# Optimization experiments

Measured on AMD Instinct MI355X. Metric: run time of the kernel, lower is better.

## Reference

```python
import jax, jax.numpy as jnp
import numpy as np

DIM = 1024
N_HEADS = 16
HEAD_DIM = DIM // N_HEADS


def setup_inputs() -> dict:
    key = jax.random.key(0)
    k_x, k_qkv, k_out = jax.random.split(key, 3)
    B, T = 4, 2048
    x = jax.random.normal(k_x, (B, T, DIM), dtype=jnp.float32)
    W_qkv = jax.random.normal(k_qkv, (DIM, 3 * DIM), dtype=jnp.float32) * 0.02
    b_qkv = jnp.zeros((3 * DIM,), dtype=jnp.float32)
    W_out = jax.random.normal(k_out, (DIM, DIM), dtype=jnp.float32) * 0.02
    b_out = jnp.zeros((DIM,), dtype=jnp.float32)
    return {"x": x, "W_qkv": W_qkv, "b_qkv": b_qkv, "W_out": W_out, "b_out": b_out}


def reference(x, W_qkv, b_qkv, W_out, b_out):
    B, T, C = x.shape
    qkv = x @ W_qkv + b_qkv  # (B, T, 3C)
    q, k, v = jnp.split(qkv, 3, axis=-1)
    # (B, H, T, D)
    q = q.reshape(B, T, N_HEADS, HEAD_DIM).transpose(0, 2, 1, 3)
    k = k.reshape(B, T, N_HEADS, HEAD_DIM).transpose(0, 2, 1, 3)
    v = v.reshape(B, T, N_HEADS, HEAD_DIM).transpose(0, 2, 1, 3)
    scale = 1.0 / jnp.sqrt(jnp.asarray(HEAD_DIM, dtype=x.dtype))
    scores = jnp.einsum('bhqd,bhkd->bhqk', q, k) * scale  # (B, H, T, T)
    causal = jnp.tril(jnp.ones((T, T), dtype=bool))  # True = allowed
    scores = jnp.where(causal, scores, jnp.asarray(-jnp.inf, dtype=scores.dtype))
    attn = jax.nn.softmax(scores, axis=-1)
    out = jnp.einsum('bhqk,bhkd->bhqd', attn, v)  # (B, H, T, D)
    out = out.transpose(0, 2, 1, 3).reshape(B, T, C)
    return out @ W_out + b_out
```

## Files before the change

kernel.cpp:

```cpp
#include <hip/hip_runtime.h>
#include <hip/hip_bf16.h>
#include <cstdint>
#include <cstddef>

#define DIM   1024
#define NH    16
#define HD    64
#define BB    4
#define TT    2048

typedef __attribute__((ext_vector_type(8))) short bf16x8;
typedef __attribute__((ext_vector_type(4))) short bf16x4;
typedef __attribute__((ext_vector_type(4))) float f32x4;
typedef __attribute__((ext_vector_type(4))) unsigned short u16x4;
typedef unsigned short u16;
typedef unsigned int u32;

#define NEG_INF (-__builtin_inff())
#define QSCALE 0.18033688011110543f
#define AS1 __attribute__((address_space(1)))
#define AS3 __attribute__((address_space(3)))

static __device__ __forceinline__ u16 f2bf(float f) {
  union { float f; unsigned u; } v; v.f = f;
  return (u16)((v.u + 0x7FFFu + ((v.u >> 16) & 1u)) >> 16);
}

static __device__ __forceinline__ u16 bfbits(float a) {
  union { __hip_bfloat16 h; u16 u; } c; c.h = __float2bfloat16(a); return c.u;
}
static __device__ __forceinline__ u32 pk_bf16(float a, float b) {
  return (u32)bfbits(a) | ((u32)bfbits(b) << 16);
}

static __device__ __forceinline__ float exp2_fast(float x) {
  float r;
  asm("v_exp_f32 %0, %1" : "=v"(r) : "v"(x));
  return r;
}

static __device__ __forceinline__ bf16x4 tr16(u32 byte_addr) {
  bf16x4 d;
  asm volatile("ds_read_b64_tr_b16 %0, %1" : "=v"(d) : "v"(byte_addr));
  return d;
}

#define MFMA16(A, B, C) __builtin_amdgcn_mfma_f32_16x16x32_bf16(A, B, C, 0, 0, 0)

__global__ __launch_bounds__(256) void k_cvt(const float* __restrict__ in,
                                             u16* __restrict__ out, int n4) {
  int i = blockIdx.x * 256 + threadIdx.x;
  if (i >= n4) return;
  float4 v = reinterpret_cast<const float4*>(in)[i];
  u16x4 o = { f2bf(v.x), f2bf(v.y), f2bf(v.z), f2bf(v.w) };
  *reinterpret_cast<u16x4*>(out + (size_t)i * 4) = o;
}

__global__ __launch_bounds__(256) void k_transpose(const float* __restrict__ in,
                                                   u16* __restrict__ out,
                                                   int R, int C) {
  __shared__ float tile[32][33];
  int bx = blockIdx.x * 32;
  int by = blockIdx.y * 32;
  int tx = threadIdx.x & 31, ty = threadIdx.x >> 5;
  #pragma unroll
  for (int i = 0; i < 32; i += 8)
    tile[ty + i][tx] = in[(size_t)(by + ty + i) * C + bx + tx];
  __syncthreads();
  #pragma unroll
  for (int i = 0; i < 32; i += 8)
    out[(size_t)(bx + ty + i) * R + by + tx] = f2bf(tile[tx][ty + i]);
}

template <int OUT_BF16>
__global__ __launch_bounds__(512, 2) void k_gemm8p(const u16* __restrict__ A,
                                                   const u16* __restrict__ Bt,
                                                   const float* __restrict__ bias,
                                                   u16* __restrict__ Cb,
                                                   float* __restrict__ Cf,
                                                   int M, int N, int K,
                                                   int scale_cols, float scale,
                                                   int nbx) {
  __shared__ __align__(16) char lds[131072];

  const int tid = threadIdx.x;
  const int nwg = gridDim.x;
  const int qq = nwg >> 3, rm = nwg & 7;
  const int xcd = blockIdx.x & 7, lidx = blockIdx.x >> 3;
  const int swz = (xcd < rm ? xcd * (qq + 1) : rm * (qq + 1) + (xcd - rm) * qq) + lidx;
  const int m0 = (swz / nbx) * 256, n0 = (swz % nbx) * 128;

  const int w = tid >> 6, lane = tid & 63;
  const int g = lane >> 4, r = lane & 15;
  const int wm = w >> 1, wn = w & 1;

  f32x4 acc[4][4] = {};
  const int KT = K >> 6;

  auto stageH = [&](char* base, const u16* src, int grow0, int kt) {
    #pragma unroll
    for (int i = 0; i < 2; ++i) {
      int o = (tid + i * 512) * 16;
      int l = o ^ (((o >> 9) & 1) << 5);
      int row = (l >> 6) & 127, ks = l >> 13, kb = l & 63;
      const u16* gp = src + (size_t)(grow0 + row) * K + kt * 64 + ks * 32 + (kb >> 1);
      __builtin_amdgcn_global_load_lds((const AS1 void*)gp, (AS3 void*)(base + o), 16, 0, 0);
    }
  };
  auto stageA = [&](int t) {
    char* ab = lds + (t % 3) * 32768;
    stageH(ab, A, m0, t);
    stageH(ab + 16384, A, m0 + 128, t);
  };
  auto stageB = [&](int t) {
    stageH(lds + 98304 + (t & 1) * 16384, Bt, n0, t);
  };

  auto ldAf = [&](int t, int f, bf16x8 (&dst)[2]) {
    const char* base = lds + (t % 3) * 32768 + (wm >> 1) * 16384;
    int rowb = ((wm & 1) * 64 + f * 16 + r) * 64 + g * 16;
    #pragma unroll
    for (int ks = 0; ks < 2; ++ks) {
      int l = ks * 8192 + rowb;
      dst[ks] = *(const bf16x8*)(base + (l ^ (((l >> 9) & 1) << 5)));
    }
  };
  auto ldBf = [&](int t, int c, bf16x8 (&dst)[2]) {
    const char* base = lds + 98304 + (t & 1) * 16384;
    int rowb = (wn * 64 + c * 16 + r) * 64 + g * 16;
    #pragma unroll
    for (int ks = 0; ks < 2; ++ks) {
      int l = ks * 8192 + rowb;
      dst[ks] = *(const bf16x8*)(base + (l ^ (((l >> 9) & 1) << 5)));
    }
  };

  stageA(0); stageB(0); stageA(1); stageB(1);
  asm volatile("s_waitcnt vmcnt(6)" ::: "memory");
  __builtin_amdgcn_s_barrier();

  for (int t = 0; t < KT; ++t) {
    const bool st = (t + 2 < KT);
    bf16x8 a0[2], a1[2], a2[2], a3[2], b0[2], b1[2], b2[2], b3[2];
    ldAf(t, 0, a0); ldAf(t, 1, a1);
    ldBf(t, 0, b0); ldBf(t, 1, b1); ldBf(t, 2, b2); ldBf(t, 3, b3);
    if (st) stageA(t + 2);
    __builtin_amdgcn_s_barrier();
    __builtin_amdgcn_s_setprio(1);
    #pragma unroll
    for (int ks = 0; ks < 2; ++ks) {
      acc[0][0] = MFMA16(a0[ks], b0[ks], acc[0][0]);
      acc[0][1] = MFMA16(a0[ks], b1[ks], acc[0][1]);
      acc[0][2] = MFMA16(a0[ks], b2[ks], acc[0][2]);
      acc[0][3] = MFMA16(a0[ks], b3[ks], acc[0][3]);
      acc[1][0] = MFMA16(a1[ks], b0[ks], acc[1][0]);
      acc[1][1] = MFMA16(a1[ks], b1[ks], acc[1][1]);
      acc[1][2] = MFMA16(a1[ks], b2[ks], acc[1][2]);
      acc[1][3] = MFMA16(a1[ks], b3[ks], acc[1][3]);
    }
    __builtin_amdgcn_s_setprio(0);
    __builtin_amdgcn_s_barrier();
    ldAf(t, 2, a2); ldAf(t, 3, a3);
    if (st) stageB(t + 2);
    __builtin_amdgcn_s_barrier();
    __builtin_amdgcn_s_setprio(1);
    #pragma unroll
    for (int ks = 0; ks < 2; ++ks) {
      acc[2][0] = MFMA16(a2[ks], b0[ks], acc[2][0]);
      acc[2][1] = MFMA16(a2[ks], b1[ks], acc[2][1]);
      acc[2][2] = MFMA16(a2[ks], b2[ks], acc[2][2]);
      acc[2][3] = MFMA16(a2[ks], b3[ks], acc[2][3]);
      acc[3][0] = MFMA16(a3[ks], b0[ks], acc[3][0]);
      acc[3][1] = MFMA16(a3[ks], b1[ks], acc[3][1]);
      acc[3][2] = MFMA16(a3[ks], b2[ks], acc[3][2]);
      acc[3][3] = MFMA16(a3[ks], b3[ks], acc[3][3]);
    }
    __builtin_amdgcn_s_setprio(0);
    if (st) asm volatile("s_waitcnt vmcnt(6)" ::: "memory");
    else    asm volatile("s_waitcnt vmcnt(0)" ::: "memory");
    __builtin_amdgcn_s_barrier();
  }

  #pragma unroll
  for (int c = 0; c < 4; ++c) {
    int col = n0 + wn * 64 + c * 16 + r;
    float bv = bias[col];
    float sc = (col < scale_cols) ? scale : 1.0f;
    #pragma unroll
    for (int f = 0; f < 4; ++f) {
      #pragma unroll
      for (int e = 0; e < 4; ++e) {
        int row = m0 + wm * 64 + f * 16 + g * 4 + e;
        float val = (acc[f][c][e] + bv) * sc;
        if (OUT_BF16) Cb[(size_t)row * N + col] = f2bf(val);
        else          Cf[(size_t)row * N + col] = val;
      }
    }
  }
}

#define KVB 64
#define LBUF16 8192

__global__ __launch_bounds__(256, 2) void k_attn(const u16* __restrict__ qkv,
                                                 u16* __restrict__ aout) {
  __shared__ __align__(16) u16 smem[2 * LBUF16];

  const int bid = blockIdx.x;
  const int swz = (bid & 7) * 64 + (bid >> 3);
  const int bh = swz >> 3;
  const int p = swz & 7;
  const int b = bh >> 4, h = bh & 15;
  const int tid = threadIdx.x, w = tid >> 6, lane = tid & 63;
  const int g = lane >> 4, r = lane & 15;

  const u32 vls0 = (u32)(uintptr_t)(AS3 u16*)(smem + 4096);
  const u32 vls1 = (u32)(uintptr_t)(AS3 u16*)(smem + LBUF16 + 4096);

  auto issueKV = [&](int buf, int t) {
    const int kv0 = t * KVB;
    u16* kb = &smem[buf * LBUF16];
    u16* vb = &smem[buf * LBUF16 + 4096];
    #pragma unroll
    for (int i = 0; i < 2; ++i) {
      int s = tid + 256 * i;
      int row = s >> 3, c8 = s & 7;
      int colg = c8 ^ (row & 7);
      const u16* gp = qkv + ((size_t)(b * TT) + kv0 + row) * (3 * DIM) + DIM + h * HD + colg * 8;
      __builtin_amdgcn_global_load_lds((const AS1 void*)gp,
                                       (AS3 void*)(kb + (size_t)s * 8), 16, 0, 0);
    }
    #pragma unroll
    for (int i = 0; i < 2; ++i) {
      int s = tid + 256 * i;
      int key = (s >> 1) & 63;
      int c = ((s >> 7) << 1) | (s & 1);
      const u16* gp = qkv + ((size_t)(b * TT) + kv0 + key) * (3 * DIM) + 2 * DIM + h * HD + c * 8;
      __builtin_amdgcn_global_load_lds((const AS1 void*)gp,
                                       (AS3 void*)(vb + (size_t)s * 8), 16, 0, 0);
    }
  };

  for (int half = 0; half < 2; ++half) {
    const int qt = half ? p : (15 - p);
    const int qbase = qt * 128;
    const int nt = 2 * qt + 2;
    const int qg0 = qbase + w * 16 + r;

    bf16x8 qf[2][2];
    #pragma unroll
    for (int qb = 0; qb < 2; ++qb) {
      const u16* qp = qkv + ((size_t)(b * TT) + qg0 + qb * 64) * (3 * DIM) + h * HD;
      #pragma unroll
      for (int kk = 0; kk < 2; ++kk)
        qf[qb][kk] = *(const bf16x8*)&qp[kk * 32 + g * 8];
    }

    f32x4 o[2][4] = {};
    float mrow[2] = { NEG_INF, NEG_INF };
    float lrow[2] = { 0.f, 0.f };

    issueKV(0, 0);
    issueKV(1, 1);
    __syncthreads();

    int cur = 0;
    for (int t = 0; t < nt; ++t) {
      const bool last = (t == nt - 1);
      const bool pen  = (t == nt - 2);
      const bool do0  = !last;
      const int kv0 = t * KVB;
      const u16* lk = &smem[cur * LBUF16];

      f32x4 s0[4] = {}, s1[4] = {};
      __builtin_amdgcn_s_setprio(1);
      #pragma unroll
      for (int c = 0; c < 4; ++c) {
        const int row = c * 16 + r;
        const int sw = (r & 7) << 3;
        bf16x8 kf0 = *(const bf16x8*)&lk[(row * 64 + g * 8) ^ sw];
        bf16x8 kf1 = *(const bf16x8*)&lk[(row * 64 + 32 + g * 8) ^ sw];
        if (do0) {
          s0[c] = MFMA16(kf0, qf[0][0], s0[c]);
          s0[c] = MFMA16(kf1, qf[0][1], s0[c]);
        }
        s1[c] = MFMA16(kf0, qf[1][0], s1[c]);
        s1[c] = MFMA16(kf1, qf[1][1], s1[c]);
      }
      __builtin_amdgcn_s_setprio(0);

      bf16x8 pf0[2], pf1[2];
      auto softmax = [&](f32x4* s, float& mref, float& lref, f32x4* ov,
                         bf16x8* pf, bool msk, int qg) {
        float pv[16];
        #pragma unroll
        for (int c = 0; c < 4; ++c)
          #pragma unroll
          for (int e = 0; e < 4; ++e) {
            float sv = s[c][e];
            if (msk) {
              int key = kv0 + c * 16 + g * 4 + e;
              if (key > qg) sv = NEG_INF;
            }
            pv[c * 4 + e] = sv;
          }
        float t8[8];
        #pragma unroll
        for (int i = 0; i < 8; ++i) t8[i] = fmaxf(pv[i], pv[i + 8]);
        #pragma unroll
        for (int i = 0; i < 4; ++i) t8[i] = fmaxf(t8[i], t8[i + 4]);
        float tm = fmaxf(fmaxf(t8[0], t8[1]), fmaxf(t8[2], t8[3]));
        tm = fmaxf(tm, __shfl_xor(tm, 16));
        tm = fmaxf(tm, __shfl_xor(tm, 32));
        if (__any(tm > mref + 8.0f)) {
          float mn = fmaxf(mref, tm);
          float corr = exp2_fast(mref - mn);
          lref *= corr;
          #pragma unroll
          for (int cd = 0; cd < 4; ++cd) ov[cd] *= corr;
          mref = mn;
        }
        #pragma unroll
        for (int i = 0; i < 16; ++i) pv[i] = exp2_fast(pv[i] - mref);
        float a8[8];
        #pragma unroll
        for (int i = 0; i < 8; ++i) a8[i] = pv[i] + pv[i + 8];
        #pragma unroll
        for (int i = 0; i < 4; ++i) a8[i] = a8[i] + a8[i + 4];
        float ps = (a8[0] + a8[1]) + (a8[2] + a8[3]);
        ps += __shfl_xor(ps, 16);
        ps += __shfl_xor(ps, 32);
        lref += ps;
        union { bf16x8 v; u32 w[4]; } u0, u1;
        #pragma unroll
        for (int k = 0; k < 4; ++k) {
          u0.w[k] = pk_bf16(pv[2 * k], pv[2 * k + 1]);
          u1.w[k] = pk_bf16(pv[8 + 2 * k], pv[9 + 2 * k]);
        }
        pf[0] = u0.v; pf[1] = u1.v;
      };
      if (do0) softmax(s0, mrow[0], lrow[0], o[0], pf0, pen, qg0);
      softmax(s1, mrow[1], lrow[1], o[1], pf1, last, qg0 + 64);

      bf16x4 tr[4][4];
      const u32 vb = (cur ? vls1 : vls0) + (u32)lane * 8;
      #pragma unroll
      for (int cd = 0; cd < 4; ++cd)
        #pragma unroll
        for (int kh = 0; kh < 4; ++kh)
          tr[cd][kh] = tr16(vb + cd * 2048 + kh * 512);
      asm volatile("s_waitcnt lgkmcnt(0)" ::: "memory");
      __builtin_amdgcn_sched_barrier(0);
      __builtin_amdgcn_s_setprio(1);
      #pragma unroll
      for (int cd = 0; cd < 4; ++cd) {
        #pragma unroll
        for (int ks = 0; ks < 2; ++ks) {
          bf16x4 lo = tr[cd][ks * 2], hi = tr[cd][ks * 2 + 1];
          bf16x8 av = { lo[0], lo[1], lo[2], lo[3], hi[0], hi[1], hi[2], hi[3] };
          if (do0) o[0][cd] = MFMA16(av, pf0[ks], o[0][cd]);
          o[1][cd] = MFMA16(av, pf1[ks], o[1][cd]);
        }
      }
      __builtin_amdgcn_s_setprio(0);

      __syncthreads();
      if (t + 2 < nt) issueKV(cur, t + 2);
      cur ^= 1;
    }

    #pragma unroll
    for (int qb = 0; qb < 2; ++qb) {
      const float inv = 1.0f / lrow[qb];
      u16* op = aout + ((size_t)(b * TT) + qg0 + qb * 64) * DIM + h * HD;
      #pragma unroll
      for (int cd = 0; cd < 4; ++cd) {
        union { u16x4 v; u32 w[2]; } pk;
        pk.w[0] = pk_bf16(o[qb][cd][0] * inv, o[qb][cd][1] * inv);
        pk.w[1] = pk_bf16(o[qb][cd][2] * inv, o[qb][cd][3] * inv);
        *(u16x4*)&op[cd * 16 + g * 4] = pk.v;
      }
    }
  }
}

extern "C" void kernel_launch(void* const* d_in, const int* in_sizes, int n_in,
                              void* d_out, int out_size, void* d_ws, size_t ws_size,
                              hipStream_t stream) {
  const float* x    = (const float*)d_in[0];
  const float* Wqkv = (const float*)d_in[1];
  const float* bqkv = (const float*)d_in[2];
  const float* Wout = (const float*)d_in[3];
  const float* bout = (const float*)d_in[4];
  float* out = (float*)d_out;

  const int M = BB * TT;
  u16* xb   = (u16*)d_ws;
  u16* wqt  = xb + (size_t)M * DIM;
  u16* wot  = wqt + (size_t)3 * DIM * DIM;
  u16* qkvb = wot + (size_t)DIM * DIM;
  u16* aob  = qkvb + (size_t)M * 3 * DIM;

  k_cvt<<<(M * DIM / 4 + 255) / 256, 256, 0, stream>>>(x, xb, M * DIM / 4);
  k_transpose<<<dim3(3 * DIM / 32, DIM / 32), 256, 0, stream>>>(Wqkv, wqt, DIM, 3 * DIM);
  k_transpose<<<dim3(DIM / 32, DIM / 32), 256, 0, stream>>>(Wout, wot, DIM, DIM);

  k_gemm8p<1><<<(M / 256) * (3 * DIM / 128), 512, 0, stream>>>(
      xb, wqt, bqkv, qkvb, nullptr, M, 3 * DIM, DIM, DIM, QSCALE, 3 * DIM / 128);

  k_attn<<<BB * NH * 8, 256, 0, stream>>>(qkvb, aob);

  k_gemm8p<0><<<(M / 256) * (DIM / 128), 512, 0, stream>>>(
      aob, wot, bout, nullptr, out, M, DIM, DIM, 0, 1.0f, DIM / 128);
}
```

Before: 169.5 us.

## Split attention block across 8 waves with one 16-row query tile each

The attention kernel now launches 512 threads per block, and each wave owns a single 16-row query slice instead of two, so 8 waves cover the 128-row tile. K/V tile loads are spread over the doubled thread count, so each thread issues one async load per operand. The per-wave register footprint halves, which allows a higher waves-per-SIMD hint and more latency hiding. In exchange there are more waves contending at each barrier, and on the last KV tile the lower four waves sit idle.

Result: slower. 175.2 us (+3.4%).

```diff
diff --git a/kernel.cpp b/kernel.cpp
--- a/kernel.cpp
+++ b/kernel.cpp
@@ -202,7 +202,7 @@
 #define KVB 64
 #define LBUF16 8192
 
-__global__ __launch_bounds__(256, 2) void k_attn(const u16* __restrict__ qkv,
+__global__ __launch_bounds__(512, 4) void k_attn(const u16* __restrict__ qkv,
                                                  u16* __restrict__ aout) {
   __shared__ __align__(16) u16 smem[2 * LBUF16];
 
@@ -221,18 +221,16 @@
     const int kv0 = t * KVB;
     u16* kb = &smem[buf * LBUF16];
     u16* vb = &smem[buf * LBUF16 + 4096];
-    #pragma unroll
-    for (int i = 0; i < 2; ++i) {
-      int s = tid + 256 * i;
+    {
+      int s = tid;
       int row = s >> 3, c8 = s & 7;
       int colg = c8 ^ (row & 7);
       const u16* gp = qkv + ((size_t)(b * TT) + kv0 + row) * (3 * DIM) + DIM + h * HD + colg * 8;
       __builtin_amdgcn_global_load_lds((const AS1 void*)gp,
                                        (AS3 void*)(kb + (size_t)s * 8), 16, 0, 0);
     }
-    #pragma unroll
-    for (int i = 0; i < 2; ++i) {
-      int s = tid + 256 * i;
+    {
+      int s = tid;
       int key = (s >> 1) & 63;
       int c = ((s >> 7) << 1) | (s & 1);
       const u16* gp = qkv + ((size_t)(b * TT) + kv0 + key) * (3 * DIM) + 2 * DIM + h * HD + c * 8;
@@ -245,20 +243,18 @@
     const int qt = half ? p : (15 - p);
     const int qbase = qt * 128;
     const int nt = 2 * qt + 2;
-    const int qg0 = qbase + w * 16 + r;
-
-    bf16x8 qf[2][2];
-    #pragma unroll
-    for (int qb = 0; qb < 2; ++qb) {
-      const u16* qp = qkv + ((size_t)(b * TT) + qg0 + qb * 64) * (3 * DIM) + h * HD;
+    const int qg = qbase + w * 16 + r;
+
+    bf16x8 qf[2];
+    {
+      const u16* qp = qkv + ((size_t)(b * TT) + qg) * (3 * DIM) + h * HD;
       #pragma unroll
       for (int kk = 0; kk < 2; ++kk)
-        qf[qb][kk] = *(const bf16x8*)&qp[kk * 32 + g * 8];
-    }
-
-    f32x4 o[2][4] = {};
-    float mrow[2] = { NEG_INF, NEG_INF };
-    float lrow[2] = { 0.f, 0.f };
+        qf[kk] = *(const bf16x8*)&qp[kk * 32 + g * 8];
+    }
+
+    f32x4 o[4] = {};
+    float mrow = NEG_INF, lrow = 0.f;
 
     issueKV(0, 0);
     issueKV(1, 1);
@@ -267,31 +263,25 @@
     int cur = 0;
     for (int t = 0; t < nt; ++t) {
       const bool last = (t == nt - 1);
-      const bool pen  = (t == nt - 2);
-      const bool do0  = !last;
+      const bool active = !(last && w < 4);
+      const bool msk = (w < 4) ? (t == nt - 2) : last;
       const int kv0 = t * KVB;
       const u16* lk = &smem[cur * LBUF16];
 
-      f32x4 s0[4] = {}, s1[4] = {};
-      __builtin_amdgcn_s_setprio(1);
-      #pragma unroll
-      for (int c = 0; c < 4; ++c) {
-        const int row = c * 16 + r;
-        const int sw = (r & 7) << 3;
-        bf16x8 kf0 = *(const bf16x8*)&lk[(row * 64 + g * 8) ^ sw];
-        bf16x8 kf1 = *(const bf16x8*)&lk[(row * 64 + 32 + g * 8) ^ sw];
-        if (do0) {
-          s0[c] = MFMA16(kf0, qf[0][0], s0[c]);
-          s0[c] = MFMA16(kf1, qf[0][1], s0[c]);
+      if (active) {
+        f32x4 s[4] = {};
+        __builtin_amdgcn_s_setprio(1);
+        #pragma unroll
+        for (int c = 0; c < 4; ++c) {
+          const int row = c * 16 + r;
+          const int sw = (r & 7) << 3;
+          bf16x8 kf0 = *(const bf16x8*)&lk[(row * 64 + g * 8) ^ sw];
+          bf16x8 kf1 = *(const bf16x8*)&lk[(row * 64 + 32 + g * 8) ^ sw];
+          s[c] = MFMA16(kf0, qf[0], s[c]);
+          s[c] = MFMA16(kf1, qf[1], s[c]);
         }
-        s1[c] = MFMA16(kf0, qf[1][0], s1[c]);
-        s1[c] = MFMA16(kf1, qf[1][1], s1[c]);
-      }
-      __builtin_amdgcn_s_setprio(0);
-
-      bf16x8 pf0[2], pf1[2];
-      auto softmax = [&](f32x4* s, float& mref, float& lref, f32x4* ov,
-                         bf16x8* pf, bool msk, int qg) {
+        __builtin_amdgcn_s_setprio(0);
+
         float pv[16];
         #pragma unroll
         for (int c = 0; c < 4; ++c)
@@ -312,16 +302,16 @@
         float tm = fmaxf(fmaxf(t8[0], t8[1]), fmaxf(t8[2], t8[3]));
         tm = fmaxf(tm, __shfl_xor(tm, 16));
         tm = fmaxf(tm, __shfl_xor(tm, 32));
-        if (__any(tm > mref + 8.0f)) {
-          float mn = fmaxf(mref, tm);
-          float corr = exp2_fast(mref - mn);
-          lref *= corr;
+        if (__any(tm > mrow + 8.0f)) {
+          float mn = fmaxf(mrow, tm);
+          float corr = exp2_fast(mrow - mn);
+          lrow *= corr;
           #pragma unroll
-          for (int cd = 0; cd < 4; ++cd) ov[cd] *= corr;
-          mref = mn;
+          for (int cd = 0; cd < 4; ++cd) o[cd] *= corr;
+          mrow = mn;
         }
         #pragma unroll
-        for (int i = 0; i < 16; ++i) pv[i] = exp2_fast(pv[i] - mref);
+        for (int i = 0; i < 16; ++i) pv[i] = exp2_fast(pv[i] - mrow);
         float a8[8];
         #pragma unroll
         for (int i = 0; i < 8; ++i) a8[i] = pv[i] + pv[i + 8];
@@ -330,54 +320,51 @@
         float ps = (a8[0] + a8[1]) + (a8[2] + a8[3]);
         ps += __shfl_xor(ps, 16);
         ps += __shfl_xor(ps, 32);
-        lref += ps;
-        union { bf16x8 v; u32 w[4]; } u0, u1;
+        lrow += ps;
+        bf16x8 pf[2];
+        union { bf16x8 v; u32 wd[4]; } u0, u1;
         #pragma unroll
         for (int k = 0; k < 4; ++k) {
-          u0.w[k] = pk_bf16(pv[2 * k], pv[2 * k + 1]);
-          u1.w[k] = pk_bf16(pv[8 + 2 * k], pv[9 + 2 * k]);
+          u0.wd[k] = pk_bf16(pv[2 * k], pv[2 * k + 1]);
+          u1.wd[k] = pk_bf16(pv[8 + 2 * k], pv[9 + 2 * k]);
         }
         pf[0] = u0.v; pf[1] = u1.v;
-      };
-      if (do0) softmax(s0, mrow[0], lrow[0], o[0], pf0, pen, qg0);
-      softmax(s1, mrow[1], lrow[1], o[1], pf1, last, qg0 + 64);
-
-      bf16x4 tr[4][4];
-      const u32 vb = (cur ? vls1 : vls0) + (u32)lane * 8;
-      #pragma unroll
-      for (int cd = 0; cd < 4; ++cd)
-        #pragma unroll
-        for (int kh = 0; kh < 4; ++kh)
-          tr[cd][kh] = tr16(vb + cd * 2048 + kh * 512);
-      asm volatile("s_waitcnt lgkmcnt(0)" ::: "memory");
-      __builtin_amdgcn_sched_barrier(0);
-      __builtin_amdgcn_s_setprio(1);
-      #pragma unroll
-      for (int cd = 0; cd < 4; ++cd) {
-        #pragma unroll
-        for (int ks = 0; ks < 2; ++ks) {
-          bf16x4 lo = tr[cd][ks * 2], hi = tr[cd][ks * 2 + 1];
-          bf16x8 av = { lo[0], lo[1], lo[2], lo[3], hi[0], hi[1], hi[2], hi[3] };
-          if (do0) o[0][cd] = MFMA16(av, pf0[ks], o[0][cd]);
-          o[1][cd] = MFMA16(av, pf1[ks], o[1][cd]);
+
+        bf16x4 tr[4][4];
+        const u32 vb = (cur ? vls1 : vls0) + (u32)lane * 8;
+        #pragma unroll
+        for (int cd = 0; cd < 4; ++cd)
+          #pragma unroll
+          for (int kh = 0; kh < 4; ++kh)
+            tr[cd][kh] = tr16(vb + cd * 2048 + kh * 512);
+        asm volatile("s_waitcnt lgkmcnt(0)" ::: "memory");
+        __builtin_amdgcn_sched_barrier(0);
+        __builtin_amdgcn_s_setprio(1);
+        #pragma unroll
+        for (int cd = 0; cd < 4; ++cd) {
+          #pragma unroll
+          for (int ks = 0; ks < 2; ++ks) {
+            bf16x4 lo = tr[cd][ks * 2], hi = tr[cd][ks * 2 + 1];
+            bf16x8 av = { lo[0], lo[1], lo[2], lo[3], hi[0], hi[1], hi[2], hi[3] };
+            o[cd] = MFMA16(av, pf[ks], o[cd]);
+          }
         }
+        __builtin_amdgcn_s_setprio(0);
       }
-      __builtin_amdgcn_s_setprio(0);
 
       __syncthreads();
       if (t + 2 < nt) issueKV(cur, t + 2);
       cur ^= 1;
     }
 
-    #pragma unroll
-    for (int qb = 0; qb < 2; ++qb) {
-      const float inv = 1.0f / lrow[qb];
-      u16* op = aout + ((size_t)(b * TT) + qg0 + qb * 64) * DIM + h * HD;
+    {
+      const float inv = 1.0f / lrow;
+      u16* op = aout + ((size_t)(b * TT) + qg) * DIM + h * HD;
       #pragma unroll
       for (int cd = 0; cd < 4; ++cd) {
-        union { u16x4 v; u32 w[2]; } pk;
-        pk.w[0] = pk_bf16(o[qb][cd][0] * inv, o[qb][cd][1] * inv);
-        pk.w[1] = pk_bf16(o[qb][cd][2] * inv, o[qb][cd][3] * inv);
+        union { u16x4 v; u32 wd[2]; } pk;
+        pk.wd[0] = pk_bf16(o[cd][0] * inv, o[cd][1] * inv);
+        pk.wd[1] = pk_bf16(o[cd][2] * inv, o[cd][3] * inv);
         *(u16x4*)&op[cd * 16 + g * 4] = pk.v;
       }
     }
@@ -408,7 +395,7 @@
   k_gemm8p<1><<<(M / 256) * (3 * DIM / 128), 512, 0, stream>>>(
       xb, wqt, bqkv, qkvb, nullptr, M, 3 * DIM, DIM, DIM, QSCALE, 3 * DIM / 128);
 
-  k_attn<<<BB * NH * 8, 256, 0, stream>>>(qkvb, aob);
+  k_attn<<<BB * NH * 8, 512, 0, stream>>>(qkvb, aob);
 
   k_gemm8p<0><<<(M / 256) * (DIM / 128), 512, 0, stream>>>(
       aob, wot, bout, nullptr, out, M, DIM, DIM, 0, 1.0f, DIM / 128);
```

## Double KV tile to 128 keys with two sub-steps per barrier

Applied to the files above, without the earlier changes.

The attention kernel now loads 128 keys per KV tile, doubling the LDS buffers, and processes each tile as two 64-key sub-steps. This halves the number of __syncthreads and async load rounds per query block. Global load addresses are precomputed per thread to cut address arithmetic. The row-sum cross-lane shuffle reduction moves out of the inner loop to the end of the block. The larger LDS footprint (64KB per block) may limit occupancy at 2 blocks per CU.

After: 170.2 us. Within noise of the previous version (+0.4%).

```diff
diff --git a/kernel.cpp b/kernel.cpp
--- a/kernel.cpp
+++ b/kernel.cpp
@@ -199,8 +199,8 @@
   }
 }
 
-#define KVB 64
-#define LBUF16 8192
+#define KVB 128
+#define LBUF16 16384
 
 __global__ __launch_bounds__(256, 2) void k_attn(const u16* __restrict__ qkv,
                                                  u16* __restrict__ aout) {
@@ -214,43 +214,44 @@
   const int tid = threadIdx.x, w = tid >> 6, lane = tid & 63;
   const int g = lane >> 4, r = lane & 15;
 
-  const u32 vls0 = (u32)(uintptr_t)(AS3 u16*)(smem + 4096);
-  const u32 vls1 = (u32)(uintptr_t)(AS3 u16*)(smem + LBUF16 + 4096);
+  const int krow0 = tid >> 3;
+  const int kcol = ((tid & 7) ^ (krow0 & 7)) * 8;
+  const int vkey0 = (tid >> 1) & 63;
+  const int vcol = (((tid >> 7) << 1) | (tid & 1)) * 8;
+  const u16* gQ = qkv + (size_t)(b * TT) * (3 * DIM) + h * HD;
+  const u16* kthr = gQ + DIM + (size_t)krow0 * (3 * DIM) + kcol;
+  const u16* vthr = gQ + 2 * DIM + (size_t)vkey0 * (3 * DIM) + vcol;
+
+  const u32 lds_base = (u32)(uintptr_t)(AS3 u16*)smem;
 
   auto issueKV = [&](int buf, int t) {
-    const int kv0 = t * KVB;
     u16* kb = &smem[buf * LBUF16];
-    u16* vb = &smem[buf * LBUF16 + 4096];
-    #pragma unroll
-    for (int i = 0; i < 2; ++i) {
-      int s = tid + 256 * i;
-      int row = s >> 3, c8 = s & 7;
-      int colg = c8 ^ (row & 7);
-      const u16* gp = qkv + ((size_t)(b * TT) + kv0 + row) * (3 * DIM) + DIM + h * HD + colg * 8;
-      __builtin_amdgcn_global_load_lds((const AS1 void*)gp,
-                                       (AS3 void*)(kb + (size_t)s * 8), 16, 0, 0);
-    }
-    #pragma unroll
-    for (int i = 0; i < 2; ++i) {
-      int s = tid + 256 * i;
-      int key = (s >> 1) & 63;
-      int c = ((s >> 7) << 1) | (s & 1);
-      const u16* gp = qkv + ((size_t)(b * TT) + kv0 + key) * (3 * DIM) + 2 * DIM + h * HD + c * 8;
-      __builtin_amdgcn_global_load_lds((const AS1 void*)gp,
-                                       (AS3 void*)(vb + (size_t)s * 8), 16, 0, 0);
+    u16* vb = &smem[buf * LBUF16 + 8192];
+    const size_t toff = (size_t)t * (KVB * 3 * DIM);
+    const u16* kt = kthr + toff;
+    const u16* vt = vthr + toff;
+    #pragma unroll
+    for (int i = 0; i < 4; ++i)
+      __builtin_amdgcn_global_load_lds(
+          (const AS1 void*)(kt + (size_t)i * 32 * 3 * DIM),
+          (AS3 void*)(kb + tid * 8 + i * 2048), 16, 0, 0);
+    #pragma unroll
+    for (int i = 0; i < 4; ++i) {
+      const u16* src = vt + (size_t)(i >> 1) * 64 * 3 * DIM + (i & 1) * 32;
+      u16* dst = vb + (i >> 1) * 4096 + tid * 8 + (i & 1) * 2048;
+      __builtin_amdgcn_global_load_lds((const AS1 void*)src, (AS3 void*)dst, 16, 0, 0);
     }
   };
 
   for (int half = 0; half < 2; ++half) {
     const int qt = half ? p : (15 - p);
-    const int qbase = qt * 128;
-    const int nt = 2 * qt + 2;
-    const int qg0 = qbase + w * 16 + r;
+    const int nt = qt + 1;
+    const int qg0 = qt * 128 + w * 16 + r;
 
     bf16x8 qf[2][2];
     #pragma unroll
     for (int qb = 0; qb < 2; ++qb) {
-      const u16* qp = qkv + ((size_t)(b * TT) + qg0 + qb * 64) * (3 * DIM) + h * HD;
+      const u16* qp = gQ + (size_t)(qg0 + qb * 64) * (3 * DIM);
       #pragma unroll
       for (int kk = 0; kk < 2; ++kk)
         qf[qb][kk] = *(const bf16x8*)&qp[kk * 32 + g * 8];
@@ -261,123 +262,133 @@
     float lrow[2] = { 0.f, 0.f };
 
     issueKV(0, 0);
-    issueKV(1, 1);
+    if (nt > 1) issueKV(1, 1);
     __syncthreads();
 
-    int cur = 0;
     for (int t = 0; t < nt; ++t) {
-      const bool last = (t == nt - 1);
-      const bool pen  = (t == nt - 2);
-      const bool do0  = !last;
-      const int kv0 = t * KVB;
-      const u16* lk = &smem[cur * LBUF16];
-
-      f32x4 s0[4] = {}, s1[4] = {};
-      __builtin_amdgcn_s_setprio(1);
+      const bool diag = (t == nt - 1);
+      const u16* lk = &smem[(t & 1) * LBUF16];
+      const u32 vbyte = lds_base + (t & 1) * (LBUF16 * 2) + 8192 * 2;
+      const int sw = (r & 7) << 3;
+
       #pragma unroll
-      for (int c = 0; c < 4; ++c) {
-        const int row = c * 16 + r;
-        const int sw = (r & 7) << 3;
-        bf16x8 kf0 = *(const bf16x8*)&lk[(row * 64 + g * 8) ^ sw];
-        bf16x8 kf1 = *(const bf16x8*)&lk[(row * 64 + 32 + g * 8) ^ sw];
-        if (do0) {
-          s0[c] = MFMA16(kf0, qf[0][0], s0[c]);
-          s0[c] = MFMA16(kf1, qf[0][1], s0[c]);
+      for (int st = 0; st < 2; ++st) {
+        const bool skip0 = diag && (st == 1);
+        const bool m0 = diag && (st == 0);
+        const bool m1 = diag && (st == 1);
+        const int k0 = t * KVB + st * 64;
+
+        bf16x8 kf[4][2];
+        #pragma unroll
+        for (int c = 0; c < 4; ++c) {
+          const int row = st * 64 + c * 16 + r;
+          kf[c][0] = *(const bf16x8*)&lk[(row * 64 + g * 8) ^ sw];
+          kf[c][1] = *(const bf16x8*)&lk[(row * 64 + 32 + g * 8) ^ sw];
         }
-        s1[c] = MFMA16(kf0, qf[1][0], s1[c]);
-        s1[c] = MFMA16(kf1, qf[1][1], s1[c]);
+        f32x4 s0[4] = {}, s1[4] = {};
+        __builtin_amdgcn_s_setprio(1);
+        #pragma unroll
+        for (int c = 0; c < 4; ++c) {
+          if (!skip0) {
+            s0[c] = MFMA16(kf[c][0], qf[0][0], s0[c]);
+            s0[c] = MFMA16(kf[c][1], qf[0][1], s0[c]);
+          }
+          s1[c] = MFMA16(kf[c][0], qf[1][0], s1[c]);
+          s1[c] = MFMA16(kf[c][1], qf[1][1], s1[c]);
+        }
+        __builtin_amdgcn_s_setprio(0);
+
+        bf16x4 tr[4][4];
+        const u32 vs = vbyte + st * 8192 + (u32)lane * 8;
+        #pragma unroll
+        for (int cd = 0; cd < 4; ++cd)
+          #pragma unroll
+          for (int kh = 0; kh < 4; ++kh)
+            tr[cd][kh] = tr16(vs + cd * 2048 + kh * 512);
+
+        bf16x8 pf0[2], pf1[2];
+        auto softmax = [&](f32x4* s, float& mref, float& lref, f32x4* ov,
+                           bf16x8* pf, bool msk, int qg) {
+          float pv[16];
+          #pragma unroll
+          for (int c = 0; c < 4; ++c)
+            #pragma unroll
+            for (int e = 0; e < 4; ++e)
+              pv[c * 4 + e] = s[c][e];
+          if (msk) {
+            #pragma unroll
+            for (int c = 0; c < 4; ++c)
+              #pragma unroll
+              for (int e = 0; e < 4; ++e)
+                if (k0 + c * 16 + g * 4 + e > qg) pv[c * 4 + e] = NEG_INF;
+          }
+          float t8[8];
+          #pragma unroll
+          for (int i = 0; i < 8; ++i) t8[i] = fmaxf(pv[i], pv[i + 8]);
+          #pragma unroll
+          for (int i = 0; i < 4; ++i) t8[i] = fmaxf(t8[i], t8[i + 4]);
+          float tm = fmaxf(fmaxf(t8[0], t8[1]), fmaxf(t8[2], t8[3]));
+          tm = fmaxf(tm, __shfl_xor(tm, 16));
+          tm = fmaxf(tm, __shfl_xor(tm, 32));
+          if (__any(tm > mref + 8.0f)) {
+            float mn = fmaxf(mref, tm);
+            float corr = exp2_fast(mref - mn);
+            lref *= corr;
+            #pragma unroll
+            for (int cd = 0; cd < 4; ++cd) ov[cd] *= corr;
+            mref = mn;
+          }
+          #pragma unroll
+          for (int i = 0; i < 16; ++i) pv[i] = exp2_fast(pv[i] - mref);
+          float a8[8];
+          #pragma unroll
+          for (int i = 0; i < 8; ++i) a8[i] = pv[i] + pv[i + 8];
+          #pragma unroll
+          for (int i = 0; i < 4; ++i) a8[i] = a8[i] + a8[i + 4];
+          lref += (a8[0] + a8[1]) + (a8[2] + a8[3]);
+          union { bf16x8 v; u32 wd[4]; } u0, u1;
+          #pragma unroll
+          for (int k = 0; k < 4; ++k) {
+            u0.wd[k] = pk_bf16(pv[2 * k], pv[2 * k + 1]);
+            u1.wd[k] = pk_bf16(pv[8 + 2 * k], pv[9 + 2 * k]);
+          }
+          pf[0] = u0.v; pf[1] = u1.v;
+        };
+        if (!skip0) softmax(s0, mrow[0], lrow[0], o[0], pf0, m0, qg0);
+        softmax(s1, mrow[1], lrow[1], o[1], pf1, m1, qg0 + 64);
+
+        asm volatile("s_waitcnt lgkmcnt(0)" ::: "memory");
+        __builtin_amdgcn_sched_barrier(0);
+        __builtin_amdgcn_s_setprio(1);
+        #pragma unroll
+        for (int cd = 0; cd < 4; ++cd) {
+          #pragma unroll
+          for (int ks = 0; ks < 2; ++ks) {
+            bf16x4 lo = tr[cd][ks * 2], hi = tr[cd][ks * 2 + 1];
+            bf16x8 av = { lo[0], lo[1], lo[2], lo[3], hi[0], hi[1], hi[2], hi[3] };
+            if (!skip0) o[0][cd] = MFMA16(av, pf0[ks], o[0][cd]);
+            o[1][cd] = MFMA16(av, pf1[ks], o[1][cd]);
+          }
+        }
+        __builtin_amdgcn_s_setprio(0);
       }
-      __builtin_amdgcn_s_setprio(0);
-
-      bf16x8 pf0[2], pf1[2];
-      auto softmax = [&](f32x4* s, float& mref, float& lref, f32x4* ov,
-                         bf16x8* pf, bool msk, int qg) {
-        float pv[16];
-        #pragma unroll
-        for (int c = 0; c < 4; ++c)
-          #pragma unroll
-          for (int e = 0; e < 4; ++e) {
-            float sv = s[c][e];
-            if (msk) {
-              int key = kv0 + c * 16 + g * 4 + e;
-              if (key > qg) sv = NEG_INF;
-            }
-            pv[c * 4 + e] = sv;
-          }
-        float t8[8];
-        #pragma unroll
-        for (int i = 0; i < 8; ++i) t8[i] = fmaxf(pv[i], pv[i + 8]);
-        #pragma unroll
-        for (int i = 0; i < 4; ++i) t8[i] = fmaxf(t8[i], t8[i + 4]);
-        float tm = fmaxf(fmaxf(t8[0], t8[1]), fmaxf(t8[2], t8[3]));
-        tm = fmaxf(tm, __shfl_xor(tm, 16));
-        tm = fmaxf(tm, __shfl_xor(tm, 32));
-        if (__any(tm > mref + 8.0f)) {
-          float mn = fmaxf(mref, tm);
-          float corr = exp2_fast(mref - mn);
-          lref *= corr;
-          #pragma unroll
-          for (int cd = 0; cd < 4; ++cd) ov[cd] *= corr;
-          mref = mn;
-        }
-        #pragma unroll
-        for (int i = 0; i < 16; ++i) pv[i] = exp2_fast(pv[i] - mref);
-        float a8[8];
-        #pragma unroll
-        for (int i = 0; i < 8; ++i) a8[i] = pv[i] + pv[i + 8];
-        #pragma unroll
-        for (int i = 0; i < 4; ++i) a8[i] = a8[i] + a8[i + 4];
-        float ps = (a8[0] + a8[1]) + (a8[2] + a8[3]);
-        ps += __shfl_xor(ps, 16);
-        ps += __shfl_xor(ps, 32);
-        lref += ps;
-        union { bf16x8 v; u32 w[4]; } u0, u1;
-        #pragma unroll
-        for (int k = 0; k < 4; ++k) {
-          u0.w[k] = pk_bf16(pv[2 * k], pv[2 * k + 1]);
-          u1.w[k] = pk_bf16(pv[8 + 2 * k], pv[9 + 2 * k]);
-        }
-        pf[0] = u0.v; pf[1] = u1.v;
-      };
-      if (do0) softmax(s0, mrow[0], lrow[0], o[0], pf0, pen, qg0);
-      softmax(s1, mrow[1], lrow[1], o[1], pf1, last, qg0 + 64);
-
-      bf16x4 tr[4][4];
-      const u32 vb = (cur ? vls1 : vls0) + (u32)lane * 8;
-      #pragma unroll
-      for (int cd = 0; cd < 4; ++cd)
-        #pragma unroll
-        for (int kh = 0; kh < 4; ++kh)
-          tr[cd][kh] = tr16(vb + cd * 2048 + kh * 512);
-      asm volatile("s_waitcnt lgkmcnt(0)" ::: "memory");
-      __builtin_amdgcn_sched_barrier(0);
-      __builtin_amdgcn_s_setprio(1);
+
+      __syncthreads();
+      if (t + 2 < nt) issueKV(t & 1, t + 2);
+    }
+
+    #pragma unroll
+    for (int qb = 0; qb < 2; ++qb) {
+      float l = lrow[qb];
+      l += __shfl_xor(l, 16);
+      l += __shfl_xor(l, 32);
+      const float inv = 1.0f / l;
+      u16* op = aout + (size_t)(b * TT + qg0 + qb * 64) * DIM + h * HD;
       #pragma unroll
       for (int cd = 0; cd < 4; ++cd) {
-        #pragma unroll
-        for (int ks = 0; ks < 2; ++ks) {
-          bf16x4 lo = tr[cd][ks * 2], hi = tr[cd][ks * 2 + 1];
-          bf16x8 av = { lo[0], lo[1], lo[2], lo[3], hi[0], hi[1], hi[2], hi[3] };
-          if (do0) o[0][cd] = MFMA16(av, pf0[ks], o[0][cd]);
-          o[1][cd] = MFMA16(av, pf1[ks], o[1][cd]);
-        }
-      }
-      __builtin_amdgcn_s_setprio(0);
-
-      __syncthreads();
-      if (t + 2 < nt) issueKV(cur, t + 2);
-      cur ^= 1;
-    }
-
-    #pragma unroll
-    for (int qb = 0; qb < 2; ++qb) {
-      const float inv = 1.0f / lrow[qb];
-      u16* op = aout + ((size_t)(b * TT) + qg0 + qb * 64) * DIM + h * HD;
-      #pragma unroll
-      for (int cd = 0; cd < 4; ++cd) {
-        union { u16x4 v; u32 w[2]; } pk;
-        pk.w[0] = pk_bf16(o[qb][cd][0] * inv, o[qb][cd][1] * inv);
-        pk.w[1] = pk_bf16(o[qb][cd][2] * inv, o[qb][cd][3] * inv);
+        union { u16x4 v; u32 wd[2]; } pk;
+        pk.wd[0] = pk_bf16(o[qb][cd][0] * inv, o[qb][cd][1] * inv);
+        pk.wd[1] = pk_bf16(o[qb][cd][2] * inv, o[qb][cd][3] * inv);
         *(u16x4*)&op[cd * 16 + g * 4] = pk.v;
       }
     }
```
